# Kernel optimization log

Measured on AMD Instinct MI355X. Metric: run time of the kernel, lower is better.

Reference implementation:

```python
import math
import jax, jax.numpy as jnp
import numpy as np

N_HEAD = 16
N_EMBD = 2048
HEAD_DIM = N_EMBD // N_HEAD  # 128
ROPE_BASE = 10000.0
EPS = 1e-12  # F.normalize eps


def setup_inputs() -> dict:
    key = jax.random.key(0)
    ks = jax.random.split(key, 5)
    B, T, C = 2, 2048, N_EMBD
    s = 0.02
    return {
        "x": jax.random.normal(ks[0], (B, T, C), jnp.float32),
        "Wq": jax.random.normal(ks[1], (C, C), jnp.float32) * s,
        "Wk": jax.random.normal(ks[2], (C, C), jnp.float32) * s,
        "Wv": jax.random.normal(ks[3], (C, C), jnp.float32) * s,
        "Wo": jax.random.normal(ks[4], (C, C), jnp.float32) * s,
        "qk_scale": jnp.ones((HEAD_DIM,), jnp.float32) / math.sqrt(N_EMBD),
    }


def _rope(x, cos, sin):
    # x: [B,T,H,D], cos/sin: [T, D/2] broadcast as [1,T,1,D/2]
    d = x.shape[-1] // 2
    x1, x2 = x[..., :d], x[..., d:]
    c = cos[None, :, None, :]
    s = sin[None, :, None, :]
    return jnp.concatenate([x1 * c + x2 * s, -x1 * s + x2 * c], axis=-1)


def reference(x, Wq, Wk, Wv, Wo, qk_scale):
    B, T, C = x.shape
    H, D = N_HEAD, HEAD_DIM

    q = (x @ Wq.T).reshape(B, T, H, D)
    k = (x @ Wk.T).reshape(B, T, H, D)
    v = (x @ Wv.T).reshape(B, T, H, D)

    # L2-normalize over head_dim, then per-channel scale (scaler() = param * sqrt(n_embd))
    scale_vec = qk_scale * math.sqrt(N_EMBD)  # == 1.0 at init
    q = scale_vec * (q / jnp.maximum(jnp.linalg.norm(q, axis=-1, keepdims=True), EPS))
    k = scale_vec * (k / jnp.maximum(jnp.linalg.norm(k, axis=-1, keepdims=True), EPS))

    # rotary embeddings (half-split, non-interleaved)
    inv_freq = 1.0 / (ROPE_BASE ** (jnp.arange(0, D, 2, dtype=jnp.float32) / D))
    freqs = jnp.arange(T, dtype=jnp.float32)[:, None] * inv_freq[None, :]  # [T, D/2]
    cos, sin = jnp.cos(freqs), jnp.sin(freqs)
    q = _rope(q, cos, sin)
    k = _rope(k, cos, sin)

    # causal SDPA with scale = sqrt(head_dim) (as in the source)
    scores = jnp.einsum("bthd,bshd->bhts", q, k) * math.sqrt(D)  # [B,H,T,T]
    causal = jnp.tril(jnp.ones((T, T), bool))
    scores = jnp.where(causal[None, None], scores, -jnp.inf)
    attn = jax.nn.softmax(scores, axis=-1)
    y = jnp.einsum("bhts,bshd->bthd", attn, v).reshape(B, T, C)
    return y @ Wo.T
```

## Files before the change

### kernel.cpp

```cpp
#include <hip/hip_runtime.h>
#include <math.h>

typedef _Float16 f16;
typedef _Float16 f16x8 __attribute__((ext_vector_type(8)));
typedef _Float16 f16x4 __attribute__((ext_vector_type(4)));
typedef float f32x4 __attribute__((ext_vector_type(4)));
typedef unsigned int u32;

#define T_ 2048
#define H_ 16
#define C_ 2048

__device__ __forceinline__ void gload_lds16(const f16* g, f16* l) {
  __builtin_amdgcn_global_load_lds((const __attribute__((address_space(1))) u32*)g,
                                   (__attribute__((address_space(3))) u32*)l, 16, 0, 0);
}

__global__ __launch_bounds__(256) void cast_all_kernel(
    const float* __restrict__ x, const float* __restrict__ wq, const float* __restrict__ wk,
    const float* __restrict__ wv, const float* __restrict__ wo,
    f16* __restrict__ xh, f16* __restrict__ wqh, f16* __restrict__ wkh,
    f16* __restrict__ wvh, f16* __restrict__ woh) {
  int b = blockIdx.x;
  const float* src; f16* dst; size_t off;
  if (b < 8192) { src = x; dst = xh; off = (size_t)b * 1024; }
  else {
    int s = (b - 8192) >> 12, bb = (b - 8192) & 4095;
    off = (size_t)bb * 1024;
    if (s == 0) { src = wq; dst = wqh; }
    else if (s == 1) { src = wk; dst = wkh; }
    else if (s == 2) { src = wv; dst = wvh; }
    else { src = wo; dst = woh; }
  }
  size_t i = off + (size_t)threadIdx.x * 4;
  float4 v = *(const float4*)&src[i];
  f16x4 o; o[0] = (f16)v.x; o[1] = (f16)v.y; o[2] = (f16)v.z; o[3] = (f16)v.w;
  *(f16x4*)&dst[i] = o;
}

template<typename OutT>
__device__ __forceinline__ void gemm128(const f16* __restrict__ A, const f16* __restrict__ Bm,
                                        OutT* __restrict__ Cm, f16* As, f16* Bs,
                                        int brow, int bcol) {
  const int K = 2048, N = 2048;
  const int tid = threadIdx.x, l = tid & 63, w = tid >> 6;
  const int lr = l & 15, lg = l >> 4;
  const int wr = (w >> 1) * 64, wc = (w & 1) * 64;
  const int srow = l >> 2, scol = (l & 3) * 8;
  const f16* gA0 = A + (size_t)(brow + w * 32 + srow) * K + scol;
  const f16* gA1 = gA0 + (size_t)16 * K;
  const f16* gB0 = Bm + (size_t)(bcol + w * 32 + srow) * K + scol;
  const f16* gB1 = gB0 + (size_t)16 * K;
  f16* lA0 = &As[(w * 32 + 0) * 32];
  f16* lA1 = &As[(w * 32 + 16) * 32];
  f16* lB0 = &Bs[(w * 32 + 0) * 32];
  f16* lB1 = &Bs[(w * 32 + 16) * 32];
  f32x4 acc[4][4] = {};
  for (int kt = 0; kt < K; kt += 32) {
    gload_lds16(gA0 + kt, lA0);
    gload_lds16(gA1 + kt, lA1);
    gload_lds16(gB0 + kt, lB0);
    gload_lds16(gB1 + kt, lB1);
    __syncthreads();
    f16x8 af[4], bf[4];
#pragma unroll
    for (int m = 0; m < 4; ++m) af[m] = *(const f16x8*)&As[(wr + m * 16 + lr) * 32 + lg * 8];
#pragma unroll
    for (int n = 0; n < 4; ++n) bf[n] = *(const f16x8*)&Bs[(wc + n * 16 + lr) * 32 + lg * 8];
#pragma unroll
    for (int m = 0; m < 4; ++m)
#pragma unroll
      for (int n = 0; n < 4; ++n)
        acc[m][n] = __builtin_amdgcn_mfma_f32_16x16x32_f16(af[m], bf[n], acc[m][n], 0, 0, 0);
    __syncthreads();
  }
#pragma unroll
  for (int m = 0; m < 4; ++m) {
    int row0 = brow + wr + m * 16 + lg * 4;
#pragma unroll
    for (int n = 0; n < 4; ++n) {
      int col = bcol + wc + n * 16 + lr;
#pragma unroll
      for (int j = 0; j < 4; ++j)
        Cm[(size_t)(row0 + j) * N + col] = (OutT)acc[m][n][j];
    }
  }
}

__global__ __launch_bounds__(256) void gemm_qkv_kernel(
    const f16* __restrict__ A, const f16* __restrict__ Wq, const f16* __restrict__ Wk,
    const f16* __restrict__ Wv, f16* __restrict__ Qo, f16* __restrict__ Ko, f16* __restrict__ Vo) {
  __shared__ f16 As[4096], Bs[4096];
  const f16* Bm; f16* Cm;
  if (blockIdx.z == 0) { Bm = Wq; Cm = Qo; }
  else if (blockIdx.z == 1) { Bm = Wk; Cm = Ko; }
  else { Bm = Wv; Cm = Vo; }
  gemm128<f16>(A, Bm, Cm, As, Bs, blockIdx.x * 128, blockIdx.y * 128);
}

__global__ __launch_bounds__(256) void gemm_out_kernel(
    const f16* __restrict__ A, const f16* __restrict__ Wo, float* __restrict__ Cm) {
  __shared__ f16 As[4096], Bs[4096];
  gemm128<float>(A, Wo, Cm, As, Bs, blockIdx.x * 128, blockIdx.y * 128);
}

__global__ __launch_bounds__(256) void normrope_kernel(f16* __restrict__ q,
                                                       const float* __restrict__ qk_scale) {
  int w = threadIdx.x >> 6, l = threadIdx.x & 63;
  int row = blockIdx.x * 4 + w;
  int t = (row >> 4) & (T_ - 1);
  size_t base = (size_t)row * 128;
  float x1 = (float)q[base + l], x2 = (float)q[base + 64 + l];
  float ss = x1 * x1 + x2 * x2;
#pragma unroll
  for (int m = 1; m < 64; m <<= 1) ss += __shfl_xor(ss, m);
  float inv = 1.0f / fmaxf(sqrtf(ss), 1e-12f);
  float sc1 = qk_scale[l] * 45.254833995939045f;
  float sc2 = qk_scale[l + 64] * 45.254833995939045f;
  float s1 = x1 * inv * sc1, s2 = x2 * inv * sc2;
  float invf = exp2f(-(float)l * 0.20762050593046013f);
  float ang = (float)t * invf;
  float sn, cs; sincosf(ang, &sn, &cs);
  float o1 = s1 * cs + s2 * sn;
  float o2 = -s1 * sn + s2 * cs;
  q[base + l] = (f16)o1;
  q[base + 64 + l] = (f16)o2;
}

__global__ __launch_bounds__(256) void attn_kernel(
    const f16* __restrict__ Q, const f16* __restrict__ K, const f16* __restrict__ V,
    f16* __restrict__ Y) {
  __shared__ f16 Ks[64 * 136];
  __shared__ f16 Vt[128 * 72];
  __shared__ f16 Ps[4 * 32 * 72];
  const int tid = threadIdx.x, l = tid & 63, w = tid >> 6;
  const int lr = l & 15, lg = l >> 4;
  const int qb = blockIdx.x * 128;
  const int bh = blockIdx.y, b = bh >> 4, h = bh & 15;
  const size_t hb = ((size_t)b * T_ * H_ + h) * 128;
  const int qw = qb + w * 32;
  f16* Pw = &Ps[w * 32 * 72];

  f16x8 qfr[2][4];
#pragma unroll
  for (int f = 0; f < 2; ++f)
#pragma unroll
    for (int dc = 0; dc < 4; ++dc)
      qfr[f][dc] = *(const f16x8*)&Q[hb + (size_t)(qw + f * 16 + lr) * 2048 + dc * 32 + lg * 8];

  float mreg[2] = {-INFINITY, -INFINITY}, rsum[2] = {0.f, 0.f};
  f32x4 acc[8][2] = {};
  const int ntiles = qb / 64 + 2;

  for (int it = 0; it < ntiles; ++it) {
    const int kv0 = it * 64;
    __syncthreads();
    {
      int row = tid >> 2, cg = (tid & 3) * 32;
      const f16* src = &K[hb + (size_t)(kv0 + row) * 2048 + cg];
      f16* dst = &Ks[row * 136 + cg];
#pragma unroll
      for (int j = 0; j < 4; ++j) *(f16x8*)(dst + j * 8) = *(const f16x8*)(src + j * 8);
    }
#pragma unroll
    for (int half = 0; half < 2; ++half) {
      int item = tid + half * 256;
      int p2 = item & 31, dg = (item >> 5) * 8;
      int kv = p2 * 2;
      const f16* s0 = &V[hb + (size_t)(kv0 + kv) * 2048 + dg];
      f16x8 r0 = *(const f16x8*)s0;
      f16x8 r1 = *(const f16x8*)(s0 + 2048);
#pragma unroll
      for (int j = 0; j < 8; ++j) {
        union { f16 f2[2]; u32 u; } pk;
        pk.f2[0] = r0[j]; pk.f2[1] = r1[j];
        *(u32*)&Vt[(dg + j) * 72 + kv] = pk.u;
      }
    }
    __syncthreads();
    if (kv0 <= qw + 31) {
#pragma unroll
      for (int f = 0; f < 2; ++f) {
        const int q = qw + f * 16 + lr;
        float p[16];
#pragma unroll
        for (int kt = 0; kt < 4; ++kt) {
          f32x4 s = {0.f, 0.f, 0.f, 0.f};
#pragma unroll
          for (int dc = 0; dc < 4; ++dc) {
            f16x8 kf = *(const f16x8*)&Ks[(kt * 16 + lr) * 136 + dc * 32 + lg * 8];
            s = __builtin_amdgcn_mfma_f32_16x16x32_f16(kf, qfr[f][dc], s, 0, 0, 0);
          }
#pragma unroll
          for (int r = 0; r < 4; ++r) {
            int kv = kv0 + kt * 16 + lg * 4 + r;
            p[kt * 4 + r] = (kv <= q) ? s[r] * 11.313708498984761f : -INFINITY;
          }
        }
        float pm = p[0];
#pragma unroll
        for (int i = 1; i < 16; ++i) pm = fmaxf(pm, p[i]);
        pm = fmaxf(pm, __shfl_xor(pm, 16));
        pm = fmaxf(pm, __shfl_xor(pm, 32));
        float mn = fmaxf(mreg[f], pm);
        float al = __expf(mreg[f] - mn);
        mreg[f] = mn;
        float sum = 0.f;
#pragma unroll
        for (int i = 0; i < 16; ++i) { p[i] = __expf(p[i] - mn); sum += p[i]; }
        sum += __shfl_xor(sum, 16);
        sum += __shfl_xor(sum, 32);
        rsum[f] = rsum[f] * al + sum;
#pragma unroll
        for (int dt = 0; dt < 8; ++dt)
#pragma unroll
          for (int j = 0; j < 4; ++j) acc[dt][f][j] *= al;
#pragma unroll
        for (int kt = 0; kt < 4; ++kt) {
          f16x4 pk;
#pragma unroll
          for (int r = 0; r < 4; ++r) pk[r] = (f16)p[kt * 4 + r];
          *(f16x4*)&Pw[(f * 16 + lr) * 72 + kt * 16 + lg * 4] = pk;
        }
      }
#pragma unroll
      for (int f = 0; f < 2; ++f) {
#pragma unroll
        for (int ks = 0; ks < 2; ++ks) {
          f16x8 pa = *(const f16x8*)&Pw[(f * 16 + lr) * 72 + ks * 32 + lg * 8];
#pragma unroll
          for (int dt = 0; dt < 8; ++dt) {
            f16x8 vf = *(const f16x8*)&Vt[(dt * 16 + lr) * 72 + ks * 32 + lg * 8];
            acc[dt][f] = __builtin_amdgcn_mfma_f32_16x16x32_f16(vf, pa, acc[dt][f], 0, 0, 0);
          }
        }
      }
    }
  }
#pragma unroll
  for (int f = 0; f < 2; ++f) {
    float inv = 1.0f / rsum[f];
    int t = qw + f * 16 + lr;
#pragma unroll
    for (int dt = 0; dt < 8; ++dt) {
      f16x4 pk;
#pragma unroll
      for (int j = 0; j < 4; ++j) pk[j] = (f16)(acc[dt][f][j] * inv);
      size_t off = ((size_t)(b * T_ + t)) * 2048 + h * 128 + dt * 16 + lg * 4;
      *(f16x4*)&Y[off] = pk;
    }
  }
}

extern "C" void kernel_launch(void* const* d_in, const int* in_sizes, int n_in,
                              void* d_out, int out_size, void* d_ws, size_t ws_size,
                              hipStream_t stream) {
  const float* x  = (const float*)d_in[0];
  const float* Wq = (const float*)d_in[1];
  const float* Wk = (const float*)d_in[2];
  const float* Wv = (const float*)d_in[3];
  const float* Wo = (const float*)d_in[4];
  const float* qk_scale = (const float*)d_in[5];
  float* out = (float*)d_out;
  char* ws = (char*)d_ws;

  f16* xh  = (f16*)(ws);
  f16* wqh = (f16*)(ws + 16777216);
  f16* wkh = (f16*)(ws + 25165824);
  f16* wvh = (f16*)(ws + 33554432);
  f16* woh = (f16*)(ws + 41943040);
  f16* qh  = (f16*)(ws + 50331648);
  f16* kh  = (f16*)(ws + 67108864);
  f16* vh  = (f16*)(ws + 83886080);
  f16* yh  = (f16*)(ws + 100663296);

  cast_all_kernel<<<dim3(24576), dim3(256), 0, stream>>>(x, Wq, Wk, Wv, Wo, xh, wqh, wkh, wvh, woh);
  gemm_qkv_kernel<<<dim3(32, 16, 3), dim3(256), 0, stream>>>(xh, wqh, wkh, wvh, qh, kh, vh);
  normrope_kernel<<<dim3(16384), dim3(256), 0, stream>>>(qh, qk_scale);
  normrope_kernel<<<dim3(16384), dim3(256), 0, stream>>>(kh, qk_scale);
  attn_kernel<<<dim3(16, 32), dim3(256), 0, stream>>>(qh, kh, vh, yh);
  gemm_out_kernel<<<dim3(32, 16), dim3(256), 0, stream>>>(yh, woh, out);
}
```

Measured before the change: 349.6 us.

## Rewrite attention with 32x32 MFMA, register P, double-buffered KV and lazy rescale

```diff
diff --git a/kernel.cpp b/kernel.cpp
--- a/kernel.cpp
+++ b/kernel.cpp
@@ -2,9 +2,12 @@
 #include <math.h>
 
 typedef _Float16 f16;
+typedef _Float16 f16x2 __attribute__((ext_vector_type(2)));
+typedef _Float16 f16x4 __attribute__((ext_vector_type(4)));
 typedef _Float16 f16x8 __attribute__((ext_vector_type(8)));
-typedef _Float16 f16x4 __attribute__((ext_vector_type(4)));
+typedef __fp16 fp16x2 __attribute__((ext_vector_type(2)));
 typedef float f32x4 __attribute__((ext_vector_type(4)));
+typedef float f32x16 __attribute__((ext_vector_type(16)));
 typedef unsigned int u32;
 
 #define T_ 2048
@@ -14,6 +17,12 @@
 __device__ __forceinline__ void gload_lds16(const f16* g, f16* l) {
   __builtin_amdgcn_global_load_lds((const __attribute__((address_space(1))) u32*)g,
                                    (__attribute__((address_space(3))) u32*)l, 16, 0, 0);
+}
+
+__device__ __forceinline__ u32 pkk(float x, float y) {
+  union { fp16x2 h; u32 u; } z;
+  z.h = __builtin_amdgcn_cvt_pkrtz(x, y);
+  return z.u;
 }
 
 __global__ __launch_bounds__(256) void cast_all_kernel(
@@ -104,9 +113,11 @@
   gemm128<float>(A, Wo, Cm, As, Bs, blockIdx.x * 128, blockIdx.y * 128);
 }
 
-__global__ __launch_bounds__(256) void normrope_kernel(f16* __restrict__ q,
+__global__ __launch_bounds__(256) void normrope_kernel(f16* __restrict__ qp, f16* __restrict__ kp,
                                                        const float* __restrict__ qk_scale) {
   int w = threadIdx.x >> 6, l = threadIdx.x & 63;
+  f16* q = blockIdx.y == 0 ? qp : kp;
+  float fac = blockIdx.y == 0 ? 512.0f : 45.254833995939045f;
   int row = blockIdx.x * 4 + w;
   int t = (row >> 4) & (T_ - 1);
   size_t base = (size_t)row * 128;
@@ -115,141 +126,173 @@
 #pragma unroll
   for (int m = 1; m < 64; m <<= 1) ss += __shfl_xor(ss, m);
   float inv = 1.0f / fmaxf(sqrtf(ss), 1e-12f);
-  float sc1 = qk_scale[l] * 45.254833995939045f;
-  float sc2 = qk_scale[l + 64] * 45.254833995939045f;
+  float sc1 = qk_scale[l] * fac;
+  float sc2 = qk_scale[l + 64] * fac;
   float s1 = x1 * inv * sc1, s2 = x2 * inv * sc2;
   float invf = exp2f(-(float)l * 0.20762050593046013f);
   float ang = (float)t * invf;
   float sn, cs; sincosf(ang, &sn, &cs);
-  float o1 = s1 * cs + s2 * sn;
-  float o2 = -s1 * sn + s2 * cs;
-  q[base + l] = (f16)o1;
-  q[base + 64 + l] = (f16)o2;
-}
-
-__global__ __launch_bounds__(256) void attn_kernel(
+  q[base + l] = (f16)(s1 * cs + s2 * sn);
+  q[base + 64 + l] = (f16)(-s1 * sn + s2 * cs);
+}
+
+#define KSTR 132
+#define VSTR 68
+__global__ __launch_bounds__(256, 2) void attn_kernel(
     const f16* __restrict__ Q, const f16* __restrict__ K, const f16* __restrict__ V,
     f16* __restrict__ Y) {
-  __shared__ f16 Ks[64 * 136];
-  __shared__ f16 Vt[128 * 72];
-  __shared__ f16 Ps[4 * 32 * 72];
+  __shared__ f16 Ks[2][64 * KSTR];
+  __shared__ f16 Vt[2][128 * VSTR];
   const int tid = threadIdx.x, l = tid & 63, w = tid >> 6;
-  const int lr = l & 15, lg = l >> 4;
-  const int qb = blockIdx.x * 128;
-  const int bh = blockIdx.y, b = bh >> 4, h = bh & 15;
+  const int lq = l & 31, hi = l >> 5;
+  const int id = blockIdx.x;
+  const int bh = id & 31;
+  const int qi = id >> 5;
+  const int qx = qi < 8 ? qi : 23 - qi;
+  const int qb = qx * 128;
+  const int b = bh >> 4, h = bh & 15;
   const size_t hb = ((size_t)b * T_ * H_ + h) * 128;
   const int qw = qb + w * 32;
-  f16* Pw = &Ps[w * 32 * 72];
-
-  f16x8 qfr[2][4];
-#pragma unroll
-  for (int f = 0; f < 2; ++f)
-#pragma unroll
-    for (int dc = 0; dc < 4; ++dc)
-      qfr[f][dc] = *(const f16x8*)&Q[hb + (size_t)(qw + f * 16 + lr) * 2048 + dc * 32 + lg * 8];
-
-  float mreg[2] = {-INFINITY, -INFINITY}, rsum[2] = {0.f, 0.f};
-  f32x4 acc[8][2] = {};
+  const int q = qw + lq;
+
+  f16x8 qB[8];
+  {
+    const f16* qp = Q + hb + (size_t)q * 2048 + hi * 8;
+#pragma unroll
+    for (int dc = 0; dc < 8; ++dc) qB[dc] = *(const f16x8*)(qp + dc * 16);
+  }
+
   const int ntiles = qb / 64 + 2;
+  const int lastit = qb / 64 + (w >> 1);
+
+  const int krow = tid >> 2, kcg = (tid & 3) * 32;
+  const int vp2 = tid & 31, vdg = (tid >> 5) * 8;
+
+  f16x8 kr0, kr1, kr2, kr3, vr0a, vr1a, vr0b, vr1b;
+  auto load_tile = [&](int kv0) {
+    const f16* ksrc = K + hb + (size_t)(kv0 + krow) * 2048 + kcg;
+    kr0 = *(const f16x8*)(ksrc);
+    kr1 = *(const f16x8*)(ksrc + 8);
+    kr2 = *(const f16x8*)(ksrc + 16);
+    kr3 = *(const f16x8*)(ksrc + 24);
+    const f16* vsrc = V + hb + (size_t)(kv0 + 2 * vp2) * 2048;
+    vr0a = *(const f16x8*)(vsrc + vdg);
+    vr1a = *(const f16x8*)(vsrc + 2048 + vdg);
+    vr0b = *(const f16x8*)(vsrc + vdg + 64);
+    vr1b = *(const f16x8*)(vsrc + 2048 + vdg + 64);
+  };
+  auto write_tile = [&](int buf) {
+    f16* kd = &Ks[buf][krow * KSTR + kcg];
+    *(f16x8*)(kd) = kr0; *(f16x8*)(kd + 8) = kr1;
+    *(f16x8*)(kd + 16) = kr2; *(f16x8*)(kd + 24) = kr3;
+#pragma unroll
+    for (int j = 0; j < 8; ++j) {
+      union { f16x2 h2; u32 u; } p0, p1;
+      p0.h2[0] = vr0a[j]; p0.h2[1] = vr1a[j];
+      *(u32*)&Vt[buf][(vdg + j) * VSTR + 2 * vp2] = p0.u;
+      p1.h2[0] = vr0b[j]; p1.h2[1] = vr1b[j];
+      *(u32*)&Vt[buf][(vdg + 64 + j) * VSTR + 2 * vp2] = p1.u;
+    }
+  };
+
+  load_tile(0);
+  write_tile(0);
+  __syncthreads();
+
+  float mreg = -INFINITY, rsum = 0.f;
+  f32x16 o0 = {}, o1 = {}, o2 = {}, o3 = {};
 
   for (int it = 0; it < ntiles; ++it) {
+    const int cur = it & 1;
     const int kv0 = it * 64;
-    __syncthreads();
-    {
-      int row = tid >> 2, cg = (tid & 3) * 32;
-      const f16* src = &K[hb + (size_t)(kv0 + row) * 2048 + cg];
-      f16* dst = &Ks[row * 136 + cg];
-#pragma unroll
-      for (int j = 0; j < 4; ++j) *(f16x8*)(dst + j * 8) = *(const f16x8*)(src + j * 8);
-    }
-#pragma unroll
-    for (int half = 0; half < 2; ++half) {
-      int item = tid + half * 256;
-      int p2 = item & 31, dg = (item >> 5) * 8;
-      int kv = p2 * 2;
-      const f16* s0 = &V[hb + (size_t)(kv0 + kv) * 2048 + dg];
-      f16x8 r0 = *(const f16x8*)s0;
-      f16x8 r1 = *(const f16x8*)(s0 + 2048);
-#pragma unroll
-      for (int j = 0; j < 8; ++j) {
-        union { f16 f2[2]; u32 u; } pk;
-        pk.f2[0] = r0[j]; pk.f2[1] = r1[j];
-        *(u32*)&Vt[(dg + j) * 72 + kv] = pk.u;
-      }
+    const bool havenext = (it + 1 < ntiles);
+    if (havenext) load_tile(kv0 + 64);
+
+    if (it <= lastit) {
+      f32x16 s0 = {}, s1 = {};
+      const f16* kb = &Ks[cur][lq * KSTR + hi * 8];
+#pragma unroll
+      for (int dc = 0; dc < 8; ++dc) {
+        f16x8 kf = *(const f16x8*)(kb + dc * 16);
+        s0 = __builtin_amdgcn_mfma_f32_32x32x16_f16(kf, qB[dc], s0, 0, 0, 0);
+      }
+      const f16* kb1 = kb + 32 * KSTR;
+#pragma unroll
+      for (int dc = 0; dc < 8; ++dc) {
+        f16x8 kf = *(const f16x8*)(kb1 + dc * 16);
+        s1 = __builtin_amdgcn_mfma_f32_32x32x16_f16(kf, qB[dc], s1, 0, 0, 0);
+      }
+      if (it == lastit) {
+#pragma unroll
+        for (int r = 0; r < 16; ++r) {
+          int crow = (r & 3) + 8 * (r >> 2) + 4 * hi;
+          s0[r] = (kv0 + crow <= q) ? s0[r] : -INFINITY;
+          s1[r] = (kv0 + 32 + crow <= q) ? s1[r] : -INFINITY;
+        }
+      }
+      float pm = s0[0];
+#pragma unroll
+      for (int r = 1; r < 16; ++r) pm = fmaxf(pm, s0[r]);
+#pragma unroll
+      for (int r = 0; r < 16; ++r) pm = fmaxf(pm, s1[r]);
+      pm = fmaxf(pm, __shfl_xor(pm, 32));
+      if (__any(pm > mreg + 8.0f)) {
+        float mn = fmaxf(mreg, pm);
+        float al = __expf(mreg - mn);
+        o0 *= al; o1 *= al; o2 *= al; o3 *= al;
+        rsum *= al; mreg = mn;
+      }
+      float sum = 0.f;
+#pragma unroll
+      for (int r = 0; r < 16; ++r) { float e = __expf(s0[r] - mreg); s0[r] = e; sum += e; }
+#pragma unroll
+      for (int r = 0; r < 16; ++r) { float e = __expf(s1[r] - mreg); s1[r] = e; sum += e; }
+      sum += __shfl_xor(sum, 32);
+      rsum += sum;
+#define PVSTEP(SV, BB, KS)                                                          \
+      {                                                                             \
+        u32 a0 = pkk(SV[8*BB+0], SV[8*BB+1]);                                       \
+        u32 a1 = pkk(SV[8*BB+2], SV[8*BB+3]);                                       \
+        u32 b0 = pkk(SV[8*BB+4], SV[8*BB+5]);                                       \
+        u32 b1 = pkk(SV[8*BB+6], SV[8*BB+7]);                                       \
+        u32 r0 = __shfl_xor(hi ? a0 : b0, 32);                                      \
+        u32 r1 = __shfl_xor(hi ? a1 : b1, 32);                                      \
+        union { u32 u[4]; f16x8 v; } pf;                                            \
+        pf.u[0] = hi ? r0 : a0; pf.u[1] = hi ? r1 : a1;                             \
+        pf.u[2] = hi ? b0 : r0; pf.u[3] = hi ? b1 : r1;                             \
+        const f16* vb = &Vt[cur][lq * VSTR + (KS) * 16 + hi * 8];                   \
+        o0 = __builtin_amdgcn_mfma_f32_32x32x16_f16(*(const f16x8*)(vb), pf.v, o0, 0, 0, 0); \
+        o1 = __builtin_amdgcn_mfma_f32_32x32x16_f16(*(const f16x8*)(vb + 32 * VSTR), pf.v, o1, 0, 0, 0); \
+        o2 = __builtin_amdgcn_mfma_f32_32x32x16_f16(*(const f16x8*)(vb + 64 * VSTR), pf.v, o2, 0, 0, 0); \
+        o3 = __builtin_amdgcn_mfma_f32_32x32x16_f16(*(const f16x8*)(vb + 96 * VSTR), pf.v, o3, 0, 0, 0); \
+      }
+      PVSTEP(s0, 0, 0)
+      PVSTEP(s0, 1, 1)
+      PVSTEP(s1, 0, 2)
+      PVSTEP(s1, 1, 3)
+#undef PVSTEP
     }
     __syncthreads();
-    if (kv0 <= qw + 31) {
-#pragma unroll
-      for (int f = 0; f < 2; ++f) {
-        const int q = qw + f * 16 + lr;
-        float p[16];
-#pragma unroll
-        for (int kt = 0; kt < 4; ++kt) {
-          f32x4 s = {0.f, 0.f, 0.f, 0.f};
-#pragma unroll
-          for (int dc = 0; dc < 4; ++dc) {
-            f16x8 kf = *(const f16x8*)&Ks[(kt * 16 + lr) * 136 + dc * 32 + lg * 8];
-            s = __builtin_amdgcn_mfma_f32_16x16x32_f16(kf, qfr[f][dc], s, 0, 0, 0);
-          }
-#pragma unroll
-          for (int r = 0; r < 4; ++r) {
-            int kv = kv0 + kt * 16 + lg * 4 + r;
-            p[kt * 4 + r] = (kv <= q) ? s[r] * 11.313708498984761f : -INFINITY;
-          }
-        }
-        float pm = p[0];
-#pragma unroll
-        for (int i = 1; i < 16; ++i) pm = fmaxf(pm, p[i]);
-        pm = fmaxf(pm, __shfl_xor(pm, 16));
-        pm = fmaxf(pm, __shfl_xor(pm, 32));
-        float mn = fmaxf(mreg[f], pm);
-        float al = __expf(mreg[f] - mn);
-        mreg[f] = mn;
-        float sum = 0.f;
-#pragma unroll
-        for (int i = 0; i < 16; ++i) { p[i] = __expf(p[i] - mn); sum += p[i]; }
-        sum += __shfl_xor(sum, 16);
-        sum += __shfl_xor(sum, 32);
-        rsum[f] = rsum[f] * al + sum;
-#pragma unroll
-        for (int dt = 0; dt < 8; ++dt)
-#pragma unroll
-          for (int j = 0; j < 4; ++j) acc[dt][f][j] *= al;
-#pragma unroll
-        for (int kt = 0; kt < 4; ++kt) {
-          f16x4 pk;
-#pragma unroll
-          for (int r = 0; r < 4; ++r) pk[r] = (f16)p[kt * 4 + r];
-          *(f16x4*)&Pw[(f * 16 + lr) * 72 + kt * 16 + lg * 4] = pk;
-        }
-      }
-#pragma unroll
-      for (int f = 0; f < 2; ++f) {
-#pragma unroll
-        for (int ks = 0; ks < 2; ++ks) {
-          f16x8 pa = *(const f16x8*)&Pw[(f * 16 + lr) * 72 + ks * 32 + lg * 8];
-#pragma unroll
-          for (int dt = 0; dt < 8; ++dt) {
-            f16x8 vf = *(const f16x8*)&Vt[(dt * 16 + lr) * 72 + ks * 32 + lg * 8];
-            acc[dt][f] = __builtin_amdgcn_mfma_f32_16x16x32_f16(vf, pa, acc[dt][f], 0, 0, 0);
-          }
-        }
-      }
+    if (havenext) {
+      write_tile(cur ^ 1);
+      __syncthreads();
     }
   }
-#pragma unroll
-  for (int f = 0; f < 2; ++f) {
-    float inv = 1.0f / rsum[f];
-    int t = qw + f * 16 + lr;
-#pragma unroll
-    for (int dt = 0; dt < 8; ++dt) {
-      f16x4 pk;
-#pragma unroll
-      for (int j = 0; j < 4; ++j) pk[j] = (f16)(acc[dt][f][j] * inv);
-      size_t off = ((size_t)(b * T_ + t)) * 2048 + h * 128 + dt * 16 + lg * 4;
-      *(f16x4*)&Y[off] = pk;
-    }
-  }
+
+  float inv = 1.0f / rsum;
+  const size_t yb = ((size_t)(b * T_ + q)) * 2048 + h * 128;
+#define OSTORE(OV, DT)                                                   \
+  {                                                                      \
+    _Pragma("unroll")                                                    \
+    for (int g = 0; g < 4; ++g) {                                        \
+      f16x4 pk;                                                          \
+      pk[0] = (f16)(OV[g * 4 + 0] * inv); pk[1] = (f16)(OV[g * 4 + 1] * inv); \
+      pk[2] = (f16)(OV[g * 4 + 2] * inv); pk[3] = (f16)(OV[g * 4 + 3] * inv); \
+      *(f16x4*)&Y[yb + (DT) * 32 + g * 8 + 4 * hi] = pk;                 \
+    }                                                                    \
+  }
+  OSTORE(o0, 0) OSTORE(o1, 1) OSTORE(o2, 2) OSTORE(o3, 3)
+#undef OSTORE
 }
 
 extern "C" void kernel_launch(void* const* d_in, const int* in_sizes, int n_in,
@@ -276,8 +319,7 @@
 
   cast_all_kernel<<<dim3(24576), dim3(256), 0, stream>>>(x, Wq, Wk, Wv, Wo, xh, wqh, wkh, wvh, woh);
   gemm_qkv_kernel<<<dim3(32, 16, 3), dim3(256), 0, stream>>>(xh, wqh, wkh, wvh, qh, kh, vh);
-  normrope_kernel<<<dim3(16384), dim3(256), 0, stream>>>(qh, qk_scale);
-  normrope_kernel<<<dim3(16384), dim3(256), 0, stream>>>(kh, qk_scale);
-  attn_kernel<<<dim3(16, 32), dim3(256), 0, stream>>>(qh, kh, vh, yh);
+  normrope_kernel<<<dim3(16384, 2), dim3(256), 0, stream>>>(qh, kh, qk_scale);
+  attn_kernel<<<dim3(512), dim3(256), 0, stream>>>(qh, kh, vh, yh);
   gemm_out_kernel<<<dim3(32, 16), dim3(256), 0, stream>>>(yh, woh, out);
 }
```

New measurement: 365.7 us. 1.05x slower.
